# Kernel tuning notes

Hardware: AMD Instinct MI355X
Metric: run time of the kernel (lower is better)

## Reference

```python
import math
import jax, jax.numpy as jnp
import numpy as np

T, B, E, H = 1024, 4, 1024, 16
DH = E // H
NUM_BUCKETS = 32
MAX_DISTANCE = 128


def setup_inputs() -> dict:
    key = jax.random.key(0)
    ks = jax.random.split(key, 12)
    s = 0.02
    return {
        "query": jax.random.normal(ks[0], (T, B, E), dtype=jnp.float32),
        "q_w": jax.random.normal(ks[1], (E, E), dtype=jnp.float32) * s,
        "q_b": jax.random.normal(ks[2], (E,), dtype=jnp.float32) * s,
        "k_w": jax.random.normal(ks[3], (E, E), dtype=jnp.float32) * s,
        "k_b": jax.random.normal(ks[4], (E,), dtype=jnp.float32) * s,
        "v_w": jax.random.normal(ks[5], (E, E), dtype=jnp.float32) * s,
        "v_b": jax.random.normal(ks[6], (E,), dtype=jnp.float32) * s,
        "out_w": jax.random.normal(ks[7], (E, E), dtype=jnp.float32) * s,
        "out_b": jnp.zeros((E,), dtype=jnp.float32),
        "rel_bias": jax.random.normal(ks[8], (NUM_BUCKETS, H), dtype=jnp.float32) * s,
        "grep_w": jax.random.normal(ks[9], (8, DH), dtype=jnp.float32) * s,
        "grep_b": jax.random.normal(ks[10], (8,), dtype=jnp.float32) * s,
        "grep_a": jnp.ones((1, H, 1, 1), dtype=jnp.float32),
    }


def _relative_position_buckets(qlen, klen):
    # bidirectional T5-style bucketing
    ctx = jnp.arange(qlen, dtype=jnp.int32)[:, None]
    mem = jnp.arange(klen, dtype=jnp.int32)[None, :]
    rp = mem - ctx  # [qlen, klen]
    n = NUM_BUCKETS // 2
    buckets = (rp > 0).astype(jnp.int32) * n
    arp = jnp.abs(rp)
    max_exact = n // 2
    is_small = arp < max_exact
    # guard log(0): values at arp<max_exact are never selected from the large branch
    large = max_exact + (
        jnp.log(jnp.maximum(arp, 1).astype(jnp.float32) / max_exact)
        / math.log(MAX_DISTANCE / max_exact)
        * (n - max_exact)
    ).astype(jnp.int32)
    large = jnp.minimum(large, n - 1)
    return buckets + jnp.where(is_small, arp, large)


def reference(query, q_w, q_b, k_w, k_b, v_w, v_b, out_w, out_b, rel_bias, grep_w, grep_b, grep_a):
    tgt_len, bsz, embed_dim = query.shape
    scaling = DH ** -0.5

    # relative-position bias [H, T, T]
    buckets = _relative_position_buckets(tgt_len, tgt_len)
    pos_bias = rel_bias[buckets]                     # [T, T, H]
    pos_bias = jnp.transpose(pos_bias, (2, 0, 1))    # [H, T, T]

    # GRU-style gate computed from the *unprojected* query, per head
    qh_raw = jnp.transpose(query, (1, 0, 2)).reshape(bsz, tgt_len, H, DH)
    qh_raw = jnp.transpose(qh_raw, (0, 2, 1, 3))     # [B, H, T, DH]
    g = jnp.einsum("bhtd,ed->bhte", qh_raw, grep_w) + grep_b  # [B,H,T,8]
    g = jax.nn.sigmoid(g.reshape(bsz, H, tgt_len, 2, 4).sum(-1))  # [B,H,T,2]
    gate_a, gate_b = g[..., 0:1], g[..., 1:2]        # [B,H,T,1]
    gate_a_1 = gate_a * (gate_b * grep_a - 1.0) + 2.0
    attn_bias = gate_a_1 * pos_bias[None]            # [B, H, T, T]

    # QKV projections (self-attention: k,v from query)
    q = (query @ q_w.T + q_b) * scaling
    k = query @ k_w.T + k_b
    v = query @ v_w.T + v_b
    qh = jnp.transpose(q.reshape(tgt_len, bsz, H, DH), (1, 2, 0, 3))  # [B,H,T,DH]
    kh = jnp.transpose(k.reshape(tgt_len, bsz, H, DH), (1, 2, 0, 3))
    vh = jnp.transpose(v.reshape(tgt_len, bsz, H, DH), (1, 2, 0, 3))

    scores = jnp.einsum("bhtd,bhsd->bhts", qh, kh) + attn_bias
    probs = jax.nn.softmax(scores, axis=-1)
    ctx = jnp.einsum("bhts,bhsd->bhtd", probs, vh)   # [B,H,T,DH]
    ctx = jnp.transpose(ctx, (2, 0, 1, 3)).reshape(tgt_len, bsz, embed_dim)
    out = ctx @ out_w.T + out_b                      # [T, B, E]
    return out
```

## Files before the change

### kernel.cpp

```cpp
#include <hip/hip_runtime.h>
#include <math.h>

#define T_ 1024
#define B_ 4
#define E_ 1024
#define H_ 16
#define DH_ 64

#define LOG2E 1.44269504088896f

typedef __attribute__((ext_vector_type(8))) __bf16 bf16x8;
typedef __attribute__((ext_vector_type(4))) __bf16 bf16x4;
typedef __attribute__((ext_vector_type(4))) float f32x4;

__device__ __forceinline__ __bf16 f2bf(float x){
  union { unsigned short u; __bf16 b; } cv;
  unsigned u32 = __float_as_uint(x);
  cv.u = (unsigned short)((u32 + 0x7fffu + ((u32 >> 16) & 1u)) >> 16);
  return cv.b;
}
__device__ __forceinline__ __bf16 f2bf_fast(float x){
  union { unsigned short u; __bf16 b; } cv;
  cv.u = (unsigned short)((__float_as_uint(x) + 0x8000u) >> 16);
  return cv.b;
}

__device__ __forceinline__ void glds16(const void* g, void* l){
  __builtin_amdgcn_global_load_lds(
      (__attribute__((address_space(1))) void*)(void*)g,
      (__attribute__((address_space(3))) void*)l,
      16, 0, 0);
}

__global__ __launch_bounds__(256) void prep_kernel(
    const float* __restrict__ q_w, const float* __restrict__ k_w,
    const float* __restrict__ v_w, const float* __restrict__ out_w,
    __bf16* __restrict__ wq, __bf16* __restrict__ wk,
    __bf16* __restrict__ wv, __bf16* __restrict__ wo,
    const float* __restrict__ query, const float* __restrict__ gw,
    const float* __restrict__ gb, const float* __restrict__ ga,
    float* __restrict__ gates, __bf16* __restrict__ qbf,
    const float* __restrict__ rel_bias, __bf16* __restrict__ tab)
{
  const int bid = blockIdx.x;
  const int tid = threadIdx.x;
  if (bid < 4096){
    const float* a; __bf16* o;
    switch (bid >> 10){
      case 0: a = q_w;  o = wq; break;
      case 1: a = k_w;  o = wk; break;
      case 2: a = v_w;  o = wv; break;
      default: a = out_w; o = wo; break;
    }
    int i = ((bid & 1023) * 256 + tid) * 4;
    float4 v = *(const float4*)(a + i);
    bf16x4 r;
    r[0] = f2bf(v.x); r[1] = f2bf(v.y); r[2] = f2bf(v.z); r[3] = f2bf(v.w);
    *(bf16x4*)(o + i) = r;
  } else if (bid < 4352){
    int t = (bid - 4096) * 4 + (tid >> 6);
    int bh = tid & 63;
    int h = bh & 15;
    const float* q = query + (size_t)t * E_ * B_ + bh * 64;
    __bf16* qo = qbf + (size_t)t * E_ * B_ + bh * 64;
    float g[8];
    #pragma unroll
    for (int e = 0; e < 8; e++) g[e] = gb[e];
    #pragma unroll
    for (int c = 0; c < 8; c++){
      float4 v0 = *(const float4*)(q + c * 8);
      float4 v1 = *(const float4*)(q + c * 8 + 4);
      bf16x8 o;
      o[0] = f2bf(v0.x); o[1] = f2bf(v0.y); o[2] = f2bf(v0.z); o[3] = f2bf(v0.w);
      o[4] = f2bf(v1.x); o[5] = f2bf(v1.y); o[6] = f2bf(v1.z); o[7] = f2bf(v1.w);
      *(bf16x8*)(qo + c * 8) = o;
      #pragma unroll
      for (int e = 0; e < 8; e++){
        const float* w = gw + e * 64 + c * 8;
        g[e] += v0.x * w[0] + v0.y * w[1] + v0.z * w[2] + v0.w * w[3]
              + v1.x * w[4] + v1.y * w[5] + v1.z * w[6] + v1.w * w[7];
      }
    }
    float a0 = (g[0] + g[1]) + (g[2] + g[3]);
    float a1 = (g[4] + g[5]) + (g[6] + g[7]);
    float sa = 1.f / (1.f + __expf(-a0));
    float sb = 1.f / (1.f + __expf(-a1));
    gates[bh * T_ + t] = (sa * (sb * ga[h] - 1.0f) + 2.0f) * LOG2E;
  } else {
    int tb = bid - 4352;
    int h = tb >> 3;
    int i = (tb & 7) * 256 + tid;
    if (i < 2047){
      int rp = i - 1023;
      int base = rp > 0 ? 16 : 0;
      int arp = rp < 0 ? -rp : rp;
      int off;
      if (arp < 8) off = arp;
      else {
        float val = (logf((float)arp * 0.125f) / 2.772588722239781f) * 8.0f;
        int lg = (int)val;
        off = 8 + (lg > 7 ? 7 : lg);
      }
      tab[h * 2047 + i] = f2bf(rel_bias[(base + off) * H_ + h]);
    }
  }
}

__global__ __launch_bounds__(256, 2) void gemm_qkv(
    const __bf16* __restrict__ A,
    const __bf16* __restrict__ W0, const __bf16* __restrict__ W1, const __bf16* __restrict__ W2,
    const float* __restrict__ b0, const float* __restrict__ b1, const float* __restrict__ b2,
    __bf16* out0, __bf16* out1, __bf16* out2)
{
  __shared__ __bf16 As[128 * 64];
  __shared__ __bf16 Bs[3][64 * 64];
  const int tid = threadIdx.x;
  const int lane = tid & 63, wid = tid >> 6;
  const int l15 = lane & 15, quad = lane >> 4;
  const int dd = blockIdx.x;
  const int j = dd >> 3;
  const int m0 = ((dd & 7) * 4 + (j & 3)) * 128;
  const int nt = j >> 2;
  const int n0 = nt * 64;

  f32x4 acc[3][2][4];
  #pragma unroll
  for (int z = 0; z < 3; z++)
    #pragma unroll
    for (int i = 0; i < 2; i++)
      #pragma unroll
      for (int jj = 0; jj < 4; jj++){
        acc[z][i][jj][0] = 0.f; acc[z][i][jj][1] = 0.f;
        acc[z][i][jj][2] = 0.f; acc[z][i][jj][3] = 0.f;
      }

  const int grow = lane >> 3;
  const int gcol = (((lane & 7) ^ grow) * 8);
  const int sw = (l15 & 7);

  for (int k0 = 0; k0 < E_; k0 += 64){
    __syncthreads();
    #pragma unroll
    for (int r = 0; r < 4; r++){
      int rb = wid * 32 + r * 8;
      glds16(A + (size_t)(m0 + rb + grow) * E_ + k0 + gcol, &As[rb * 64]);
    }
    #pragma unroll
    for (int r = 0; r < 2; r++){
      int rb = wid * 16 + r * 8;
      glds16(W0 + (size_t)(n0 + rb + grow) * E_ + k0 + gcol, &Bs[0][rb * 64]);
      glds16(W1 + (size_t)(n0 + rb + grow) * E_ + k0 + gcol, &Bs[1][rb * 64]);
      glds16(W2 + (size_t)(n0 + rb + grow) * E_ + k0 + gcol, &Bs[2][rb * 64]);
    }
    __syncthreads();
    #pragma unroll
    for (int kq = 0; kq < 2; kq++){
      const int ce = ((kq * 4 + quad) ^ sw) * 8;
      bf16x8 am[2];
      #pragma unroll
      for (int i = 0; i < 2; i++) am[i] = *(const bf16x8*)&As[(wid * 32 + i * 16 + l15) * 64 + ce];
      #pragma unroll
      for (int z = 0; z < 3; z++){
        bf16x8 bn[4];
        #pragma unroll
        for (int jj = 0; jj < 4; jj++) bn[jj] = *(const bf16x8*)&Bs[z][(jj * 16 + l15) * 64 + ce];
        #pragma unroll
        for (int i = 0; i < 2; i++)
          #pragma unroll
          for (int jj = 0; jj < 4; jj++)
            acc[z][i][jj] = __builtin_amdgcn_mfma_f32_16x16x32_bf16(am[i], bn[jj], acc[z][i][jj], 0, 0, 0);
      }
    }
  }

  #pragma unroll
  for (int z = 0; z < 2; z++){
    __bf16* outp = z ? out1 : out0;
    const float* bias = z ? b1 : b0;
    const float scale = z ? 1.0f : 0.125f * LOG2E;
    #pragma unroll
    for (int i = 0; i < 2; i++){
      const int row0 = m0 + wid * 32 + i * 16 + quad * 4;
      #pragma unroll
      for (int jj = 0; jj < 4; jj++){
        const int col = n0 + jj * 16 + l15;
        const float bc = bias[col];
        const int d2 = col & 63;
        #pragma unroll
        for (int r = 0; r < 4; r++){
          float v = (acc[z][i][jj][r] + bc) * scale;
          int row = row0 + r;
          int t = row >> 2, bb = row & 3;
          outp[(size_t)((bb * H_ + nt) * T_ + t) * DH_ + d2] = f2bf(v);
        }
      }
    }
  }

  __syncthreads();
  __bf16 (*vbuf)[4][32] = (__bf16 (*)[4][32])&As[0];
  #pragma unroll
  for (int i = 0; i < 2; i++){
    const int t_local = wid * 8 + i * 4 + quad;
    #pragma unroll
    for (int jj = 0; jj < 4; jj++){
      const int nl = jj * 16 + l15;
      const float bc = b2[n0 + nl];
      #pragma unroll
      for (int r = 0; r < 4; r++)
        vbuf[nl][r][t_local] = f2bf(acc[2][i][jj][r] + bc);
    }
  }
  __syncthreads();
  {
    const int nl = tid >> 2;
    const int bb = tid & 3;
    __bf16* dst = out2 + (size_t)((bb * H_ + nt) * DH_ + nl) * T_ + (m0 >> 2);
    const __bf16* src = &vbuf[nl][bb][0];
    #pragma unroll
    for (int c = 0; c < 4; c++)
      *(bf16x8*)(dst + c * 8) = *(const bf16x8*)(src + c * 8);
  }
}

__global__ __launch_bounds__(256) void gemm_out(
    const __bf16* __restrict__ A, const __bf16* __restrict__ W,
    const float* __restrict__ bias, float* __restrict__ out)
{
  __shared__ __bf16 As[64 * 64];
  __shared__ __bf16 Bs[128 * 64];
  const int tid = threadIdx.x;
  const int lane = tid & 63, wid = tid >> 6;
  const int l15 = lane & 15, quad = lane >> 4;
  const int wm = wid >> 1, wn = wid & 1;
  const int dd = blockIdx.x;
  const int j = dd >> 3;
  const int m0 = ((dd & 7) * 8 + (j & 7)) * 64;
  const int n0 = (j >> 3) * 128;

  f32x4 acc[2][4];
  #pragma unroll
  for (int i = 0; i < 2; i++)
    #pragma unroll
    for (int jj = 0; jj < 4; jj++){
      acc[i][jj][0] = 0.f; acc[i][jj][1] = 0.f; acc[i][jj][2] = 0.f; acc[i][jj][3] = 0.f;
    }

  const int grow = lane >> 3;
  const int gcol = (((lane & 7) ^ grow) * 8);
  const int sw = (l15 & 7);

  for (int k0 = 0; k0 < E_; k0 += 64){
    __syncthreads();
    #pragma unroll
    for (int r = 0; r < 2; r++){
      int rbA = wid * 16 + r * 8;
      glds16(A + (size_t)(m0 + rbA + grow) * E_ + k0 + gcol, &As[rbA * 64]);
    }
    #pragma unroll
    for (int r = 0; r < 4; r++){
      int rbB = wid * 32 + r * 8;
      glds16(W + (size_t)(n0 + rbB + grow) * E_ + k0 + gcol, &Bs[rbB * 64]);
    }
    __syncthreads();
    #pragma unroll
    for (int kq = 0; kq < 2; kq++){
      const int ce = ((kq * 4 + quad) ^ sw) * 8;
      bf16x8 am[2], bn[4];
      #pragma unroll
      for (int i = 0; i < 2; i++) am[i] = *(const bf16x8*)&As[(wm * 32 + i * 16 + l15) * 64 + ce];
      #pragma unroll
      for (int jj = 0; jj < 4; jj++) bn[jj] = *(const bf16x8*)&Bs[(wn * 64 + jj * 16 + l15) * 64 + ce];
      #pragma unroll
      for (int i = 0; i < 2; i++)
        #pragma unroll
        for (int jj = 0; jj < 4; jj++)
          acc[i][jj] = __builtin_amdgcn_mfma_f32_16x16x32_bf16(am[i], bn[jj], acc[i][jj], 0, 0, 0);
    }
  }

  #pragma unroll
  for (int i = 0; i < 2; i++){
    const int row0 = m0 + wm * 32 + i * 16 + quad * 4;
    #pragma unroll
    for (int jj = 0; jj < 4; jj++){
      const int col = n0 + wn * 64 + jj * 16 + l15;
      const float bc = bias[col];
      #pragma unroll
      for (int r = 0; r < 4; r++)
        out[(size_t)(row0 + r) * E_ + col] = acc[i][jj][r] + bc;
    }
  }
}

__global__ __launch_bounds__(256) void attn_kernel(
    const __bf16* __restrict__ qg, const __bf16* __restrict__ kg, const __bf16* __restrict__ vgT,
    const float* __restrict__ gates, const __bf16* __restrict__ tab,
    __bf16* __restrict__ ctx)
{
  const int LD = 72;
  __shared__ __bf16 Ks[64 * LD];
  __shared__ __bf16 Vt[64 * LD];
  __shared__ __bf16 Pt[4][2][16 * LD];
  __shared__ __bf16 tabh[2048];

  const int tid = threadIdx.x;
  const int lane = tid & 63, wid = tid >> 6;
  const int l15 = lane & 15, quad = lane >> 4;
  const int dgrid = blockIdx.x;
  const int jj = dgrid >> 3;
  const int bh = (dgrid & 7) + 8 * (jj & 7);
  const int tq = jj >> 3;
  const int b = bh >> 4, h = bh & 15;
  const __bf16* qb = qg + (size_t)bh * T_ * DH_;
  const __bf16* kb = kg + (size_t)bh * T_ * DH_;
  const __bf16* vb = vgT + (size_t)bh * DH_ * T_;

  for (int i = tid; i < 2047; i += 256) tabh[i] = tab[h * 2047 + i];

  const int t0w = tq * 128 + wid * 32;
  bf16x8 bq[2][2];
  float g[2];
  int ibase[2];
  #pragma unroll
  for (int tg = 0; tg < 2; tg++){
    int t_lane = t0w + tg * 16 + l15;
    bq[tg][0] = *(const bf16x8*)(qb + (size_t)t_lane * DH_ + quad * 8);
    bq[tg][1] = *(const bf16x8*)(qb + (size_t)t_lane * DH_ + 32 + quad * 8);
    g[tg] = gates[bh * T_ + t_lane];
    ibase[tg] = 1023 - t_lane;
  }

  const int r0 = tid >> 3;
  const int c0 = (tid & 7) * 8;

  float l_run[2] = {0.f, 0.f};
  f32x4 O[2][4];
  #pragma unroll
  for (int tg = 0; tg < 2; tg++)
    #pragma unroll
    for (int mt = 0; mt < 4; mt++){ O[tg][mt][0]=0.f; O[tg][mt][1]=0.f; O[tg][mt][2]=0.f; O[tg][mt][3]=0.f; }

  bf16x8 kA = *(const bf16x8*)(kb + (size_t)r0 * DH_ + c0);
  bf16x8 kB = *(const bf16x8*)(kb + (size_t)(r0 + 32) * DH_ + c0);
  bf16x8 vA = *(const bf16x8*)(vb + (size_t)r0 * T_ + c0);
  bf16x8 vB = *(const bf16x8*)(vb + (size_t)(r0 + 32) * T_ + c0);

  for (int s0 = 0; s0 < T_; s0 += 64){
    __syncthreads();
    *(bf16x8*)&Ks[r0 * LD + c0] = kA;
    *(bf16x8*)&Ks[(r0 + 32) * LD + c0] = kB;
    *(bf16x8*)&Vt[r0 * LD + c0] = vA;
    *(bf16x8*)&Vt[(r0 + 32) * LD + c0] = vB;
    __syncthreads();

    int sn = (s0 + 64) & (T_ - 1);
    kA = *(const bf16x8*)(kb + (size_t)(sn + r0) * DH_ + c0);
    kB = *(const bf16x8*)(kb + (size_t)(sn + r0 + 32) * DH_ + c0);
    vA = *(const bf16x8*)(vb + (size_t)r0 * T_ + sn + c0);
    vB = *(const bf16x8*)(vb + (size_t)(r0 + 32) * T_ + sn + c0);

    f32x4 S[2][4];
    #pragma unroll
    for (int nt = 0; nt < 4; nt++){
      bf16x8 ak0 = *(const bf16x8*)&Ks[(nt * 16 + l15) * LD + quad * 8];
      bf16x8 ak1 = *(const bf16x8*)&Ks[(nt * 16 + l15) * LD + 32 + quad * 8];
      #pragma unroll
      for (int tg = 0; tg < 2; tg++){
        f32x4 a; a[0]=0.f; a[1]=0.f; a[2]=0.f; a[3]=0.f;
        a = __builtin_amdgcn_mfma_f32_16x16x32_bf16(ak0, bq[tg][0], a, 0, 0, 0);
        a = __builtin_amdgcn_mfma_f32_16x16x32_bf16(ak1, bq[tg][1], a, 0, 0, 0);
        S[tg][nt] = a;
      }
    }

    #pragma unroll
    for (int tg = 0; tg < 2; tg++){
      const int ib = ibase[tg] + s0;
      #pragma unroll
      for (int nt = 0; nt < 4; nt++)
        #pragma unroll
        for (int r = 0; r < 4; r++)
          S[tg][nt][r] = __builtin_amdgcn_exp2f(S[tg][nt][r] + g[tg] * (float)tabh[ib + nt * 16 + quad * 4 + r]);

      __bf16* pw = &Pt[wid][tg][0];
      #pragma unroll
      for (int nt = 0; nt < 4; nt++){
        bf16x4 p;
        p[0] = f2bf_fast(S[tg][nt][0]); p[1] = f2bf_fast(S[tg][nt][1]);
        p[2] = f2bf_fast(S[tg][nt][2]); p[3] = f2bf_fast(S[tg][nt][3]);
        *(bf16x4*)&pw[l15 * LD + nt * 16 + quad * 4] = p;
      }

      float rs = 0.f;
      #pragma unroll
      for (int nt = 0; nt < 4; nt++) rs += (S[tg][nt][0] + S[tg][nt][1]) + (S[tg][nt][2] + S[tg][nt][3]);
      rs += __shfl_xor(rs, 16, 64);
      rs += __shfl_xor(rs, 32, 64);
      l_run[tg] += rs;
    }

    #pragma unroll
    for (int ks = 0; ks < 2; ks++){
      bf16x8 bp[2];
      #pragma unroll
      for (int tg = 0; tg < 2; tg++)
        bp[tg] = *(const bf16x8*)&Pt[wid][tg][l15 * LD + ks * 32 + quad * 8];
      #pragma unroll
      for (int mt = 0; mt < 4; mt++){
        bf16x8 av = *(const bf16x8*)&Vt[(mt * 16 + l15) * LD + ks * 32 + quad * 8];
        #pragma unroll
        for (int tg = 0; tg < 2; tg++)
          O[tg][mt] = __builtin_amdgcn_mfma_f32_16x16x32_bf16(av, bp[tg], O[tg][mt], 0, 0, 0);
      }
    }
  }

  #pragma unroll
  for (int tg = 0; tg < 2; tg++){
    const int t_lane = t0w + tg * 16 + l15;
    const float inv = 1.f / l_run[tg];
    #pragma unroll
    for (int mt = 0; mt < 4; mt++){
      bf16x4 o;
      o[0] = f2bf(O[tg][mt][0] * inv); o[1] = f2bf(O[tg][mt][1] * inv);
      o[2] = f2bf(O[tg][mt][2] * inv); o[3] = f2bf(O[tg][mt][3] * inv);
      *(bf16x4*)&ctx[(size_t)(t_lane * B_ + b) * E_ + h * DH_ + mt * 16 + quad * 4] = o;
    }
  }
}

extern "C" void kernel_launch(void* const* d_in, const int* in_sizes, int n_in,
                              void* d_out, int out_size, void* d_ws, size_t ws_size,
                              hipStream_t stream)
{
  (void)in_sizes; (void)n_in; (void)out_size; (void)ws_size;
  const float* query    = (const float*)d_in[0];
  const float* q_w      = (const float*)d_in[1];
  const float* q_b      = (const float*)d_in[2];
  const float* k_w      = (const float*)d_in[3];
  const float* k_b      = (const float*)d_in[4];
  const float* v_w      = (const float*)d_in[5];
  const float* v_b      = (const float*)d_in[6];
  const float* out_w    = (const float*)d_in[7];
  const float* out_b    = (const float*)d_in[8];
  const float* rel_bias = (const float*)d_in[9];
  const float* grep_w   = (const float*)d_in[10];
  const float* grep_b   = (const float*)d_in[11];
  const float* grep_a   = (const float*)d_in[12];

  char* ws = (char*)d_ws;
  size_t off = 0;
  __bf16* qbf = (__bf16*)(ws + off); off += (size_t)4096 * 1024 * 2;
  __bf16* wq  = (__bf16*)(ws + off); off += (size_t)1024 * 1024 * 2;
  __bf16* wk  = (__bf16*)(ws + off); off += (size_t)1024 * 1024 * 2;
  __bf16* wv  = (__bf16*)(ws + off); off += (size_t)1024 * 1024 * 2;
  __bf16* wo  = (__bf16*)(ws + off); off += (size_t)1024 * 1024 * 2;
  __bf16* qh  = (__bf16*)(ws + off); off += (size_t)4096 * 1024 * 2;
  __bf16* kh  = (__bf16*)(ws + off); off += (size_t)4096 * 1024 * 2;
  __bf16* vhT = (__bf16*)(ws + off); off += (size_t)4096 * 1024 * 2;
  __bf16* ctx = (__bf16*)(ws + off); off += (size_t)4096 * 1024 * 2;
  float* gates = (float*)(ws + off); off += (size_t)65536 * 4;
  __bf16* tab  = (__bf16*)(ws + off); off += (size_t)16 * 2047 * 2;

  prep_kernel<<<4480, 256, 0, stream>>>(q_w, k_w, v_w, out_w, wq, wk, wv, wo,
                                        query, grep_w, grep_b, grep_a, gates, qbf,
                                        rel_bias, tab);
  gemm_qkv<<<512, 256, 0, stream>>>(qbf, wq, wk, wv, q_b, k_b, v_b, qh, kh, vhT);
  attn_kernel<<<512, 256, 0, stream>>>(qh, kh, vhT, gates, tab, ctx);
  gemm_out<<<512, 256, 0, stream>>>(ctx, wo, out_b, (float*)d_out);
}
```

Measured before the change: 207.6 us.

## Use direct-to-LDS swizzled K/V loads, smaller attention blocks, constant-bias fast path

The attention kernel now loads K and V tiles straight into LDS with global_load_lds using an XOR-swizzled layout in place of the padded register-staged copies, and drops the register prefetch of the next tile. Blocks shrink to 128 threads covering 64 query rows, which doubles the grid. For key tiles far from the diagonal, where the relative-position bucket is constant, the bias is taken as a single scalar instead of per-element table lookups. The bias table is also kept in fp32, which costs a little more memory traffic, and losing the software prefetch may expose more load latency.

```diff
diff --git a/kernel.cpp b/kernel.cpp
--- a/kernel.cpp
+++ b/kernel.cpp
@@ -40,7 +40,7 @@
     const float* __restrict__ query, const float* __restrict__ gw,
     const float* __restrict__ gb, const float* __restrict__ ga,
     float* __restrict__ gates, __bf16* __restrict__ qbf,
-    const float* __restrict__ rel_bias, __bf16* __restrict__ tab)
+    const float* __restrict__ rel_bias, float* __restrict__ tab)
 {
   const int bid = blockIdx.x;
   const int tid = threadIdx.x;
@@ -101,7 +101,7 @@
         int lg = (int)val;
         off = 8 + (lg > 7 ? 7 : lg);
       }
-      tab[h * 2047 + i] = f2bf(rel_bias[(base + off) * H_ + h]);
+      tab[h * 2047 + i] = rel_bias[(base + off) * H_ + h];
     }
   }
 }
@@ -293,32 +293,32 @@
   }
 }
 
-__global__ __launch_bounds__(256) void attn_kernel(
+__global__ __launch_bounds__(128) void attn_kernel(
     const __bf16* __restrict__ qg, const __bf16* __restrict__ kg, const __bf16* __restrict__ vgT,
-    const float* __restrict__ gates, const __bf16* __restrict__ tab,
+    const float* __restrict__ gates, const float* __restrict__ tab,
     __bf16* __restrict__ ctx)
 {
-  const int LD = 72;
-  __shared__ __bf16 Ks[64 * LD];
-  __shared__ __bf16 Vt[64 * LD];
-  __shared__ __bf16 Pt[4][2][16 * LD];
-  __shared__ __bf16 tabh[2048];
+  const int LDP = 72;
+  __shared__ __bf16 Ks[64 * 64];
+  __shared__ __bf16 Vt[64 * 64];
+  __shared__ __bf16 Pt[2][2][16 * LDP];
+  __shared__ float tabh[2048];
 
   const int tid = threadIdx.x;
   const int lane = tid & 63, wid = tid >> 6;
   const int l15 = lane & 15, quad = lane >> 4;
   const int dgrid = blockIdx.x;
-  const int jj = dgrid >> 3;
-  const int bh = (dgrid & 7) + 8 * (jj & 7);
-  const int tq = jj >> 3;
+  const int j = dgrid >> 3;
+  const int bh = (dgrid & 7) + 8 * (j & 7);
+  const int tq = j >> 3;
   const int b = bh >> 4, h = bh & 15;
   const __bf16* qb = qg + (size_t)bh * T_ * DH_;
   const __bf16* kb = kg + (size_t)bh * T_ * DH_;
   const __bf16* vb = vgT + (size_t)bh * DH_ * T_;
 
-  for (int i = tid; i < 2047; i += 256) tabh[i] = tab[h * 2047 + i];
-
-  const int t0w = tq * 128 + wid * 32;
+  for (int i = tid; i < 2047; i += 128) tabh[i] = tab[h * 2047 + i];
+
+  const int t0w = tq * 64 + wid * 32;
   bf16x8 bq[2][2];
   float g[2];
   int ibase[2];
@@ -331,8 +331,9 @@
     ibase[tg] = 1023 - t_lane;
   }
 
-  const int r0 = tid >> 3;
-  const int c0 = (tid & 7) * 8;
+  const int grow = lane >> 3;
+  const int gcol = (((lane & 7) ^ grow) * 8);
+  const int swf = (l15 & 7);
 
   float l_run[2] = {0.f, 0.f};
   f32x4 O[2][4];
@@ -341,30 +342,22 @@
     #pragma unroll
     for (int mt = 0; mt < 4; mt++){ O[tg][mt][0]=0.f; O[tg][mt][1]=0.f; O[tg][mt][2]=0.f; O[tg][mt][3]=0.f; }
 
-  bf16x8 kA = *(const bf16x8*)(kb + (size_t)r0 * DH_ + c0);
-  bf16x8 kB = *(const bf16x8*)(kb + (size_t)(r0 + 32) * DH_ + c0);
-  bf16x8 vA = *(const bf16x8*)(vb + (size_t)r0 * T_ + c0);
-  bf16x8 vB = *(const bf16x8*)(vb + (size_t)(r0 + 32) * T_ + c0);
-
   for (int s0 = 0; s0 < T_; s0 += 64){
     __syncthreads();
-    *(bf16x8*)&Ks[r0 * LD + c0] = kA;
-    *(bf16x8*)&Ks[(r0 + 32) * LD + c0] = kB;
-    *(bf16x8*)&Vt[r0 * LD + c0] = vA;
-    *(bf16x8*)&Vt[(r0 + 32) * LD + c0] = vB;
-    __syncthreads();
-
-    int sn = (s0 + 64) & (T_ - 1);
-    kA = *(const bf16x8*)(kb + (size_t)(sn + r0) * DH_ + c0);
-    kB = *(const bf16x8*)(kb + (size_t)(sn + r0 + 32) * DH_ + c0);
-    vA = *(const bf16x8*)(vb + (size_t)r0 * T_ + sn + c0);
-    vB = *(const bf16x8*)(vb + (size_t)(r0 + 32) * T_ + sn + c0);
+    #pragma unroll
+    for (int r = 0; r < 4; r++){
+      int rb = wid * 32 + r * 8;
+      glds16(kb + (size_t)(s0 + rb + grow) * DH_ + gcol, &Ks[rb * 64]);
+      glds16(vb + (size_t)(rb + grow) * T_ + s0 + gcol, &Vt[rb * 64]);
+    }
+    __syncthreads();
 
     f32x4 S[2][4];
     #pragma unroll
     for (int nt = 0; nt < 4; nt++){
-      bf16x8 ak0 = *(const bf16x8*)&Ks[(nt * 16 + l15) * LD + quad * 8];
-      bf16x8 ak1 = *(const bf16x8*)&Ks[(nt * 16 + l15) * LD + 32 + quad * 8];
+      const int rowb = (nt * 16 + l15) * 64;
+      bf16x8 ak0 = *(const bf16x8*)&Ks[rowb + ((quad ^ swf) * 8)];
+      bf16x8 ak1 = *(const bf16x8*)&Ks[rowb + (((4 + quad) ^ swf) * 8)];
       #pragma unroll
       for (int tg = 0; tg < 2; tg++){
         f32x4 a; a[0]=0.f; a[1]=0.f; a[2]=0.f; a[3]=0.f;
@@ -374,24 +367,40 @@
       }
     }
 
+    const int drel = s0 - t0w;
+    if (drel >= 160 || drel <= -192){
+      const float sv = (drel > 0) ? tabh[1151] : tabh[895];
+      #pragma unroll
+      for (int tg = 0; tg < 2; tg++){
+        const float cb = g[tg] * sv;
+        #pragma unroll
+        for (int nt = 0; nt < 4; nt++)
+          #pragma unroll
+          for (int r = 0; r < 4; r++)
+            S[tg][nt][r] = __builtin_amdgcn_exp2f(S[tg][nt][r] + cb);
+      }
+    } else {
+      #pragma unroll
+      for (int tg = 0; tg < 2; tg++){
+        const int ib = ibase[tg] + s0;
+        #pragma unroll
+        for (int nt = 0; nt < 4; nt++)
+          #pragma unroll
+          for (int r = 0; r < 4; r++)
+            S[tg][nt][r] = __builtin_amdgcn_exp2f(S[tg][nt][r] + g[tg] * tabh[ib + nt * 16 + quad * 4 + r]);
+      }
+    }
+
     #pragma unroll
     for (int tg = 0; tg < 2; tg++){
-      const int ib = ibase[tg] + s0;
-      #pragma unroll
-      for (int nt = 0; nt < 4; nt++)
-        #pragma unroll
-        for (int r = 0; r < 4; r++)
-          S[tg][nt][r] = __builtin_amdgcn_exp2f(S[tg][nt][r] + g[tg] * (float)tabh[ib + nt * 16 + quad * 4 + r]);
-
       __bf16* pw = &Pt[wid][tg][0];
       #pragma unroll
       for (int nt = 0; nt < 4; nt++){
         bf16x4 p;
         p[0] = f2bf_fast(S[tg][nt][0]); p[1] = f2bf_fast(S[tg][nt][1]);
         p[2] = f2bf_fast(S[tg][nt][2]); p[3] = f2bf_fast(S[tg][nt][3]);
-        *(bf16x4*)&pw[l15 * LD + nt * 16 + quad * 4] = p;
-      }
-
+        *(bf16x4*)&pw[l15 * LDP + nt * 16 + quad * 4] = p;
+      }
       float rs = 0.f;
       #pragma unroll
       for (int nt = 0; nt < 4; nt++) rs += (S[tg][nt][0] + S[tg][nt][1]) + (S[tg][nt][2] + S[tg][nt][3]);
@@ -405,10 +414,11 @@
       bf16x8 bp[2];
       #pragma unroll
       for (int tg = 0; tg < 2; tg++)
-        bp[tg] = *(const bf16x8*)&Pt[wid][tg][l15 * LD + ks * 32 + quad * 8];
+        bp[tg] = *(const bf16x8*)&Pt[wid][tg][l15 * LDP + ks * 32 + quad * 8];
       #pragma unroll
       for (int mt = 0; mt < 4; mt++){
-        bf16x8 av = *(const bf16x8*)&Vt[(mt * 16 + l15) * LD + ks * 32 + quad * 8];
+        const int rowb = (mt * 16 + l15) * 64;
+        bf16x8 av = *(const bf16x8*)&Vt[rowb + (((ks * 4 + quad) ^ swf) * 8)];
         #pragma unroll
         for (int tg = 0; tg < 2; tg++)
           O[tg][mt] = __builtin_amdgcn_mfma_f32_16x16x32_bf16(av, bp[tg], O[tg][mt], 0, 0, 0);
@@ -461,12 +471,12 @@
   __bf16* vhT = (__bf16*)(ws + off); off += (size_t)4096 * 1024 * 2;
   __bf16* ctx = (__bf16*)(ws + off); off += (size_t)4096 * 1024 * 2;
   float* gates = (float*)(ws + off); off += (size_t)65536 * 4;
-  __bf16* tab  = (__bf16*)(ws + off); off += (size_t)16 * 2047 * 2;
+  float* tab   = (float*)(ws + off); off += (size_t)16 * 2047 * 4;
 
   prep_kernel<<<4480, 256, 0, stream>>>(q_w, k_w, v_w, out_w, wq, wk, wv, wo,
                                         query, grep_w, grep_b, grep_a, gates, qbf,
                                         rel_bias, tab);
   gemm_qkv<<<512, 256, 0, stream>>>(qbf, wq, wk, wv, q_b, k_b, v_b, qh, kh, vhT);
-  attn_kernel<<<512, 256, 0, stream>>>(qh, kh, vhT, gates, tab, ctx);
+  attn_kernel<<<1024, 128, 0, stream>>>(qh, kh, vhT, gates, tab, ctx);
   gemm_out<<<512, 256, 0, stream>>>(ctx, wo, out_b, (float*)d_out);
 }
```

Result: faster. 198.9 us (-4.2%).
